# Optimization experiments

Measured on AMD Instinct MI355X. Metric: run time of the kernel, lower is better.

Reference implementation:

```python
import jax, jax.numpy as jnp
import numpy as np

EPS = 1e-5
NUM_GROUPS = 32


def setup_inputs() -> dict:
    key = jax.random.key(0)
    ks = jax.random.split(key, 4)
    b, c, h, w = 8, 512, 32, 32
    x = jax.random.normal(ks[0], (b, c, h, w), dtype=jnp.float32)
    gn_weight = jnp.ones((c,), dtype=jnp.float32)
    gn_bias = jnp.zeros((c,), dtype=jnp.float32)
    qkv_w = jax.random.normal(ks[1], (3 * c, c), dtype=jnp.float32) * (1.0 / np.sqrt(c))
    qkv_b = jnp.zeros((3 * c,), dtype=jnp.float32)
    proj_w = jax.random.normal(ks[2], (c, c), dtype=jnp.float32) * (1.0 / np.sqrt(c))
    proj_b = jnp.zeros((c,), dtype=jnp.float32)
    return {"x": x, "gn_weight": gn_weight, "gn_bias": gn_bias,
            "qkv_w": qkv_w, "qkv_b": qkv_b, "proj_w": proj_w, "proj_b": proj_b}


def _group_norm(x, weight, bias):
    b, c, h, w = x.shape
    xg = x.reshape(b, NUM_GROUPS, c // NUM_GROUPS, h, w)
    mean = xg.mean(axis=(2, 3, 4), keepdims=True)
    var = xg.var(axis=(2, 3, 4), keepdims=True)
    xn = ((xg - mean) * jax.lax.rsqrt(var + EPS)).reshape(b, c, h, w)
    return xn * weight[None, :, None, None] + bias[None, :, None, None]


def reference(x, gn_weight, gn_bias, qkv_w, qkv_b, proj_w, proj_b):
    b, c, h, w = x.shape
    scale = c ** (-0.5)
    xn = _group_norm(x, gn_weight, gn_bias)
    # 1x1 conv == per-pixel matmul over channels
    qkv = jnp.einsum('bchw,oc->bohw', xn, qkv_w) + qkv_b[None, :, None, None]
    q, k, v = jnp.split(qkv.reshape(b, 3 * c, h * w), 3, axis=1)  # each [b, c, N]
    attn = jax.nn.softmax(jnp.einsum('bci,bcj->bij', q, k) * scale, axis=-1)
    out = jnp.einsum('bij,bcj->bci', attn, v).reshape(b, c, h, w)
    proj = jnp.einsum('bchw,oc->bohw', out, proj_w) + proj_b[None, :, None, None]
    return x + proj
```

## Files before the change

kernel.cpp:

```cpp
#include <hip/hip_runtime.h>
#include <cmath>

constexpr int Bsz = 8, Cch = 512, NPIX = 1024;
constexpr int NG = 32, CPG = 16;

typedef __attribute__((ext_vector_type(4))) float f32x4;
typedef __attribute__((ext_vector_type(8))) short s16x8;

#define GLOBAL_AS __attribute__((address_space(1)))
#define LDS_AS __attribute__((address_space(3)))

__device__ inline short f2bf(float f) {
  union { float f; unsigned u; } c = {f};
  unsigned r = (c.u + 0x7fffu + ((c.u >> 16) & 1u)) >> 16;
  return (short)r;
}

__device__ inline float wave_reduce_sum(float v) {
#pragma unroll
  for (int off = 32; off > 0; off >>= 1) v += __shfl_xor(v, off, 64);
  return v;
}

__global__ __launch_bounds__(256) void prep_kernel(
    const float* __restrict__ x, const float* __restrict__ w,
    const float* __restrict__ bb, short* __restrict__ xnt,
    const float* __restrict__ in1, short* __restrict__ out1, int n1,
    const float* __restrict__ in2, short* __restrict__ out2, int n2) {
  __shared__ float sm[8];
  if (blockIdx.x >= 256) {
    const int i = ((blockIdx.x - 256) * 256 + threadIdx.x) * 4;
    const float* in = in1;
    short* out = out1;
    int j = i;
    if (i >= n1) { in = in2; out = out2; j = i - n1; }
    if (j + 3 < (i >= n1 ? n2 : n1)) {
      float4 v = *(const float4*)(in + j);
      short o[4] = {f2bf(v.x), f2bf(v.y), f2bf(v.z), f2bf(v.w)};
      *(uint2*)(out + j) = *(const uint2*)o;
    }
    return;
  }
  const int bg = ((int)blockIdx.x & 7) * 32 + ((int)blockIdx.x >> 3);
  const int b = bg >> 5, g = bg & 31;
  const float* xp = x + ((size_t)(b * Cch + g * CPG)) * NPIX;
  float s = 0.f, ss = 0.f;
  for (int i = threadIdx.x * 4; i < CPG * NPIX; i += 1024) {
    float4 v = *(const float4*)(xp + i);
    s += v.x + v.y + v.z + v.w;
    ss += v.x * v.x + v.y * v.y + v.z * v.z + v.w * v.w;
  }
  s = wave_reduce_sum(s);
  ss = wave_reduce_sum(ss);
  const int wv = threadIdx.x >> 6;
  if ((threadIdx.x & 63) == 0) { sm[wv] = s; sm[4 + wv] = ss; }
  __syncthreads();
  const float tsum = sm[0] + sm[1] + sm[2] + sm[3];
  const float tsq = sm[4] + sm[5] + sm[6] + sm[7];
  const float inv_n = 1.0f / (CPG * NPIX);
  const float mean = tsum * inv_n;
  const float rstd = rsqrtf(tsq * inv_n - mean * mean + 1e-5f);
  float wc[CPG], bc[CPG];
#pragma unroll
  for (int c = 0; c < CPG; ++c) {
    wc[c] = w[g * CPG + c] * rstd;
    bc[c] = bb[g * CPG + c] - mean * wc[c];
  }
  const int p0 = threadIdx.x * 4;
  short ov[4][CPG];
#pragma unroll
  for (int c = 0; c < CPG; ++c) {
    float4 v = *(const float4*)(xp + (size_t)c * NPIX + p0);
    ov[0][c] = f2bf(v.x * wc[c] + bc[c]);
    ov[1][c] = f2bf(v.y * wc[c] + bc[c]);
    ov[2][c] = f2bf(v.z * wc[c] + bc[c]);
    ov[3][c] = f2bf(v.w * wc[c] + bc[c]);
  }
#pragma unroll
  for (int j = 0; j < 4; ++j) {
    short* op = xnt + ((size_t)(b * NPIX + p0 + j)) * Cch + g * CPG;
    *(uint4*)op = *(const uint4*)&ov[j][0];
    *(uint4*)(op + 8) = *(const uint4*)&ov[j][8];
  }
}

template <int BM, int BN, int EPI>
__global__ __launch_bounds__(256) void mfma_gemm(
    const short* __restrict__ A, const short* __restrict__ B, int K, int lda,
    int ldb, long sA, long sB, const float* __restrict__ bias, float alpha,
    void* __restrict__ Cp, long sC, int ldc, void* __restrict__ C2p, long sC2,
    const float* __restrict__ resid, long sR) {
  constexpr int FM = BM / 32, FN = BN / 32;
  constexpr int NA = BM / 64, NB = BN / 64;
  __shared__ __align__(16) short Asl[BM * 32];
  __shared__ __align__(16) short Bsl[BN * 32];
  const int t = threadIdx.x;
  const int lane = t & 63, wave = t >> 6;

  const int gx = gridDim.x, gy = gridDim.y;
  const int nwg = gx * gy * (int)gridDim.z;
  int flat = (int)blockIdx.x + gx * ((int)blockIdx.y + gy * (int)blockIdx.z);
  flat = (flat & 7) * (nwg >> 3) + (flat >> 3);
  const int bx = flat % gx;
  const int rem = flat / gx;
  const int by = rem % gy;
  const int bz = rem / gy;

  const int m0 = by * BM, n0 = bx * BN;
  A += sA * bz;
  B += sB * bz;

  const short* ga[NA];
  const short* gb[NB];
  short* la[NA];
  short* lb[NB];
#pragma unroll
  for (int i = 0; i < NA; ++i) {
    const int s = i * 256 + t;
    const int row = ((s >> 6) * 16) + (s & 15);
    const int q = (s >> 4) & 3;
    ga[i] = A + (size_t)(m0 + row) * lda + q * 8;
    la[i] = Asl + s * 8;
  }
#pragma unroll
  for (int i = 0; i < NB; ++i) {
    const int s = i * 256 + t;
    const int row = ((s >> 6) * 16) + (s & 15);
    const int q = (s >> 4) & 3;
    gb[i] = B + (size_t)(n0 + row) * ldb + q * 8;
    lb[i] = Bsl + s * 8;
  }

  f32x4 acc[FM][FN] = {};
  const int wm = wave & 1, wn = wave >> 1;

  for (int k0 = 0; k0 < K; k0 += 32) {
#pragma unroll
    for (int i = 0; i < NA; ++i) {
      __builtin_amdgcn_global_load_lds((const GLOBAL_AS void*)ga[i],
                                       (LDS_AS void*)la[i], 16, 0, 0);
      ga[i] += 32;
    }
#pragma unroll
    for (int i = 0; i < NB; ++i) {
      __builtin_amdgcn_global_load_lds((const GLOBAL_AS void*)gb[i],
                                       (LDS_AS void*)lb[i], 16, 0, 0);
      gb[i] += 32;
    }
    __syncthreads();
    s16x8 af[FM], bf[FN];
#pragma unroll
    for (int i = 0; i < FM; ++i)
      af[i] = *(const s16x8*)(Asl + (wm * FM + i) * 512 + lane * 8);
#pragma unroll
    for (int i = 0; i < FN; ++i)
      bf[i] = *(const s16x8*)(Bsl + (wn * FN + i) * 512 + lane * 8);
#pragma unroll
    for (int im = 0; im < FM; ++im)
#pragma unroll
      for (int in = 0; in < FN; ++in)
        acc[im][in] = __builtin_amdgcn_mfma_f32_16x16x32_bf16(
            af[im], bf[in], acc[im][in], 0, 0, 0);
    __syncthreads();
  }

  const int quad = lane >> 4, nn = lane & 15;
#pragma unroll
  for (int im = 0; im < FM; ++im) {
#pragma unroll
    for (int in = 0; in < FN; ++in) {
      const int m = m0 + (wm * FM + im) * 16 + quad * 4;
      const int n = n0 + (wn * FN + in) * 16 + nn;
      if (EPI == 0) {
        if (m0 < 1024) {
          short* Cq = (short*)Cp + sC * bz;
          short o[4];
#pragma unroll
          for (int r = 0; r < 4; ++r) o[r] = f2bf(acc[im][in][r] + bias[m + r]);
          *(uint2*)(Cq + (size_t)n * ldc + m) = *(const uint2*)o;
        } else {
          short* Cv = (short*)C2p + sC2 * bz;
#pragma unroll
          for (int r = 0; r < 4; ++r)
            Cv[(size_t)(m - 1024 + r) * ldc + n] =
                f2bf(acc[im][in][r] + bias[m + r]);
        }
      } else {
        float* Cf = (float*)Cp + sC * bz;
        const float* R = resid + sR * bz;
#pragma unroll
        for (int r = 0; r < 4; ++r)
          Cf[(size_t)(m + r) * ldc + n] =
              acc[im][in][r] + bias[m + r] + R[(size_t)(m + r) * ldc + n];
      }
    }
  }
}

__global__ __launch_bounds__(256, 2) void flash_kernel(
    const short* __restrict__ qkt,
    const short* __restrict__ vbuf,
    short* __restrict__ Ot) {
  __shared__ __align__(16) short Ksl[2][2048 * 8];
  __shared__ __align__(16) short Psl[2][2][16][40];
  __shared__ float lsum[2][2][16];
  const int t = threadIdx.x;
  const int lane = t & 63, wave = t >> 6;
  const int wm = wave & 1, wn = wave >> 1;
  const int nn = lane & 15, quad = lane >> 4;
  const int f = (int)blockIdx.x + 32 * (int)blockIdx.y;
  const int flat = (f & 7) * 32 + (f >> 3);
  const int b = flat >> 5;
  const int q0 = (flat & 31) * 32;
  const float scale = 0.044194173824159216f;

  s16x8 qf[16];
  {
    const short* qp =
        qkt + ((size_t)(b * 1024 + q0 + wm * 16 + nn)) * 1024 + quad * 8;
#pragma unroll
    for (int s = 0; s < 16; ++s) qf[s] = *(const s16x8*)(qp + s * 32);
  }

  const short* gk[8];
#pragma unroll
  for (int i = 0; i < 8; ++i) {
    const int cc = i * 256 + t;
    const int s = cc >> 7, h = (cc >> 6) & 1, ll = cc & 63;
    const int row = h * 16 + (ll & 15);
    const int k = s * 32 + ((ll >> 4) & 3) * 8;
    gk[i] = qkt + ((size_t)(b * 1024 + row)) * 1024 + 512 + k;
  }
  const short* vbase =
      vbuf + ((size_t)(b * 512 + wn * 256 + nn)) * 1024 + quad * 8;

  f32x4 acc_o[16] = {};
  float lp[4] = {0.f, 0.f, 0.f, 0.f};

#pragma unroll
  for (int i = 0; i < 8; ++i)
    __builtin_amdgcn_global_load_lds(
        (const GLOBAL_AS void*)gk[i],
        (LDS_AS void*)(&Ksl[0][0] + (i * 256 + t) * 8), 16, 0, 0);
  __syncthreads();

  for (int tile = 0; tile < 32; ++tile) {
    const int cur = tile & 1;
    if (tile < 31) {
#pragma unroll
      for (int i = 0; i < 8; ++i)
        __builtin_amdgcn_global_load_lds(
            (const GLOBAL_AS void*)(gk[i] + (size_t)(tile + 1) * 32 * 1024),
            (LDS_AS void*)(&Ksl[cur ^ 1][0] + (i * 256 + t) * 8), 16, 0, 0);
    }
    const short* vp = vbase + (size_t)tile * 32;
    s16x8 vf[16];
#pragma unroll
    for (int ff = 0; ff < 8; ++ff)
      vf[ff] = *(const s16x8*)(vp + (size_t)ff * 16 * 1024);
    f32x4 sa = {}, sb = {};
#pragma unroll
    for (int s = 0; s < 8; ++s) {
      s16x8 kfa = *(const s16x8*)(&Ksl[cur][0] + ((s * 2 + wn) * 64 + lane) * 8);
      s16x8 kfb =
          *(const s16x8*)(&Ksl[cur][0] + (((s + 8) * 2 + wn) * 64 + lane) * 8);
      sa = __builtin_amdgcn_mfma_f32_16x16x32_bf16(qf[s], kfa, sa, 0, 0, 0);
      sb = __builtin_amdgcn_mfma_f32_16x16x32_bf16(qf[s + 8], kfb, sb, 0, 0, 0);
    }
    f32x4 s_acc = sa + sb;
#pragma unroll
    for (int ff = 8; ff < 16; ++ff)
      vf[ff] = *(const s16x8*)(vp + (size_t)ff * 16 * 1024);
#pragma unroll
    for (int r = 0; r < 4; ++r) {
      float e = __expf(s_acc[r] * scale);
      lp[r] += e;
      Psl[cur][wm][quad * 4 + r][wn * 16 + nn] = f2bf(e);
    }
    __syncthreads();
    s16x8 pa = *(const s16x8*)(&Psl[cur][wm][0][0] + nn * 40 + quad * 8);
#pragma unroll
    for (int ff = 0; ff < 16; ++ff)
      acc_o[ff] =
          __builtin_amdgcn_mfma_f32_16x16x32_bf16(pa, vf[ff], acc_o[ff], 0, 0, 0);
  }

#pragma unroll
  for (int off = 1; off < 16; off <<= 1)
#pragma unroll
    for (int r = 0; r < 4; ++r) lp[r] += __shfl_xor(lp[r], off, 64);
  if (nn == 0) {
#pragma unroll
    for (int r = 0; r < 4; ++r) lsum[wm][wn][quad * 4 + r] = lp[r];
  }
  __syncthreads();
  float inv[4];
#pragma unroll
  for (int r = 0; r < 4; ++r) {
    const int row = quad * 4 + r;
    inv[r] = 1.0f / (lsum[wm][0][row] + lsum[wm][1][row]);
  }
  short* op = Ot + ((size_t)(b * 1024 + q0 + wm * 16 + quad * 4)) * 512 +
              wn * 256 + nn;
#pragma unroll
  for (int ff = 0; ff < 16; ++ff)
#pragma unroll
    for (int r = 0; r < 4; ++r)
      op[(size_t)r * 512 + ff * 16] = f2bf(acc_o[ff][r] * inv[r]);
}

extern "C" void kernel_launch(void* const* d_in, const int* in_sizes, int n_in,
                              void* d_out, int out_size, void* d_ws,
                              size_t ws_size, hipStream_t stream) {
  const float* x = (const float*)d_in[0];
  const float* gnw = (const float*)d_in[1];
  const float* gnb = (const float*)d_in[2];
  const float* qkvw = (const float*)d_in[3];
  const float* qkvb = (const float*)d_in[4];
  const float* projw = (const float*)d_in[5];
  const float* projb = (const float*)d_in[6];
  float* out = (float*)d_out;

  char* ws = (char*)d_ws;
  short* xnt = (short*)ws;
  short* qkt = (short*)(ws + (8ull << 20));
  short* vbuf = (short*)(ws + (24ull << 20));
  short* Ot = (short*)(ws + (32ull << 20));
  short* wq = (short*)(ws + (40ull << 20));
  short* wp = (short*)(ws + (42ull << 20));

  prep_kernel<<<1280, 256, 0, stream>>>(x, gnw, gnb, xnt, qkvw, wq, 1536 * 512,
                                        projw, wp, 512 * 512);

  mfma_gemm<128, 128, 0><<<dim3(8, 12, Bsz), 256, 0, stream>>>(
      wq, xnt, 512, 512, 512, 0L, 1024L * 512, qkvb, 1.0f, qkt, 1024L * 1024,
      1024, vbuf, 512L * 1024, nullptr, 0L);

  flash_kernel<<<dim3(32, 8), 256, 0, stream>>>(qkt, vbuf, Ot);

  mfma_gemm<64, 128, 3><<<dim3(8, 8, Bsz), 256, 0, stream>>>(
      wp, Ot, 512, 512, 512, 0L, 1024L * 512, projb, 1.0f, out, 512L * 1024,
      1024, nullptr, 0L, x, 512L * 1024);
}
```

Before: 226.0 us.

## Stage V tiles through LDS with async global_load_lds double-buffering in flash kernel

V fragments are now loaded into a double-buffered LDS tile with global_load_lds, replacing per-wave direct global vector loads. K becomes single-buffered and its next-tile prefetch is issued after the P barrier. The point is to cut register pressure from the 16 held V fragments and coalesce V traffic across the block. LDS use grows to roughly 96KB, so the occupancy hint of 2 blocks is dropped, and the K prefetch now overlaps less with compute.

```diff
diff --git a/kernel.cpp b/kernel.cpp
--- a/kernel.cpp
+++ b/kernel.cpp
@@ -197,12 +197,13 @@
   }
 }
 
-__global__ __launch_bounds__(256, 2) void flash_kernel(
+__global__ __launch_bounds__(256) void flash_kernel(
     const short* __restrict__ qkt,
     const short* __restrict__ vbuf,
     short* __restrict__ Ot) {
-  __shared__ __align__(16) short Ksl[2][2048 * 8];
-  __shared__ __align__(16) short Psl[2][2][16][40];
+  __shared__ __align__(16) short Ksl[2048 * 8];
+  __shared__ __align__(16) short Vsl[2][2048 * 8];
+  __shared__ __align__(16) short Psl[2][16][40];
   __shared__ float lsum[2][2][16];
   const int t = threadIdx.x;
   const int lane = t & 63, wave = t >> 6;
@@ -231,58 +232,68 @@
     const int k = s * 32 + ((ll >> 4) & 3) * 8;
     gk[i] = qkt + ((size_t)(b * 1024 + row)) * 1024 + 512 + k;
   }
-  const short* vbase =
-      vbuf + ((size_t)(b * 512 + wn * 256 + nn)) * 1024 + quad * 8;
+  const short* gv[8];
+#pragma unroll
+  for (int i = 0; i < 8; ++i) {
+    const int cc = i * 256 + t;
+    const int F = cc >> 6;
+    const int c = F * 16 + (cc & 15);
+    const int jq = (cc >> 4) & 3;
+    gv[i] = vbuf + ((size_t)(b * 512 + c)) * 1024 + jq * 8;
+  }
 
   f32x4 acc_o[16] = {};
   float lp[4] = {0.f, 0.f, 0.f, 0.f};
 
 #pragma unroll
-  for (int i = 0; i < 8; ++i)
+  for (int i = 0; i < 8; ++i) {
+    __builtin_amdgcn_global_load_lds((const GLOBAL_AS void*)gk[i],
+                                     (LDS_AS void*)(&Ksl[0] + (i * 256 + t) * 8),
+                                     16, 0, 0);
     __builtin_amdgcn_global_load_lds(
-        (const GLOBAL_AS void*)gk[i],
-        (LDS_AS void*)(&Ksl[0][0] + (i * 256 + t) * 8), 16, 0, 0);
-  __syncthreads();
+        (const GLOBAL_AS void*)gv[i],
+        (LDS_AS void*)(&Vsl[0][0] + (i * 256 + t) * 8), 16, 0, 0);
+  }
 
   for (int tile = 0; tile < 32; ++tile) {
-    const int cur = tile & 1;
-    if (tile < 31) {
-#pragma unroll
-      for (int i = 0; i < 8; ++i)
-        __builtin_amdgcn_global_load_lds(
-            (const GLOBAL_AS void*)(gk[i] + (size_t)(tile + 1) * 32 * 1024),
-            (LDS_AS void*)(&Ksl[cur ^ 1][0] + (i * 256 + t) * 8), 16, 0, 0);
-    }
-    const short* vp = vbase + (size_t)tile * 32;
-    s16x8 vf[16];
-#pragma unroll
-    for (int ff = 0; ff < 8; ++ff)
-      vf[ff] = *(const s16x8*)(vp + (size_t)ff * 16 * 1024);
+    const int pv = tile & 1;
+    __syncthreads();
     f32x4 sa = {}, sb = {};
 #pragma unroll
     for (int s = 0; s < 8; ++s) {
-      s16x8 kfa = *(const s16x8*)(&Ksl[cur][0] + ((s * 2 + wn) * 64 + lane) * 8);
+      s16x8 kfa = *(const s16x8*)(&Ksl[0] + ((s * 2 + wn) * 64 + lane) * 8);
       s16x8 kfb =
-          *(const s16x8*)(&Ksl[cur][0] + (((s + 8) * 2 + wn) * 64 + lane) * 8);
+          *(const s16x8*)(&Ksl[0] + (((s + 8) * 2 + wn) * 64 + lane) * 8);
       sa = __builtin_amdgcn_mfma_f32_16x16x32_bf16(qf[s], kfa, sa, 0, 0, 0);
       sb = __builtin_amdgcn_mfma_f32_16x16x32_bf16(qf[s + 8], kfb, sb, 0, 0, 0);
     }
     f32x4 s_acc = sa + sb;
-#pragma unroll
-    for (int ff = 8; ff < 16; ++ff)
-      vf[ff] = *(const s16x8*)(vp + (size_t)ff * 16 * 1024);
 #pragma unroll
     for (int r = 0; r < 4; ++r) {
       float e = __expf(s_acc[r] * scale);
       lp[r] += e;
-      Psl[cur][wm][quad * 4 + r][wn * 16 + nn] = f2bf(e);
+      Psl[wm][quad * 4 + r][wn * 16 + nn] = f2bf(e);
     }
     __syncthreads();
-    s16x8 pa = *(const s16x8*)(&Psl[cur][wm][0][0] + nn * 40 + quad * 8);
-#pragma unroll
-    for (int ff = 0; ff < 16; ++ff)
+    if (tile < 31) {
+#pragma unroll
+      for (int i = 0; i < 8; ++i) {
+        __builtin_amdgcn_global_load_lds(
+            (const GLOBAL_AS void*)(gk[i] + (size_t)(tile + 1) * 32 * 1024),
+            (LDS_AS void*)(&Ksl[0] + (i * 256 + t) * 8), 16, 0, 0);
+        __builtin_amdgcn_global_load_lds(
+            (const GLOBAL_AS void*)(gv[i] + (size_t)(tile + 1) * 32),
+            (LDS_AS void*)(&Vsl[pv ^ 1][0] + (i * 256 + t) * 8), 16, 0, 0);
+      }
+    }
+    s16x8 pa = *(const s16x8*)(&Psl[wm][0][0] + nn * 40 + quad * 8);
+#pragma unroll
+    for (int ff = 0; ff < 16; ++ff) {
+      s16x8 vf =
+          *(const s16x8*)(&Vsl[pv][0] + ((wn * 16 + ff) * 64 + lane) * 8);
       acc_o[ff] =
-          __builtin_amdgcn_mfma_f32_16x16x32_bf16(pa, vf[ff], acc_o[ff], 0, 0, 0);
+          __builtin_amdgcn_mfma_f32_16x16x32_bf16(pa, vf, acc_o[ff], 0, 0, 0);
+    }
   }
 
 #pragma unroll
```

Result: slower. 235.1 us (+4.0%).
